# Kernel optimization log

Measured on AMD Instinct MI355X. Metric: run time of the kernel, lower is better.

Reference implementation:

```python
import jax, jax.numpy as jnp
import numpy as np

BIG_NUMBER = 1e7   # repo constant used to mask padded adjacency slots
MAX_ITERS = 32     # params['flow_iters']


def _build_graph(B, N, D, valid_deg, seed=0):
    """Random d-regular-ish graph: each valid slot d holds a permutation of nodes,
    so every node has exactly `valid_deg` in-edges. in_indices[b,v,d] = (b,u,s)
    such that adj[b,u,s] == v. Padded slots (d >= valid_deg) hold the sentinel N
    and their in_indices point to a padded (near-zero-weight) flow entry."""
    rng = np.random.default_rng(seed)
    adj = np.full((B, N, D), N, dtype=np.int32)
    in_idx = np.zeros((B, N, D, 3), dtype=np.int32)
    in_idx[..., 0] = np.arange(B, dtype=np.int32)[:, None, None]
    in_idx[..., 2] = valid_deg  # padded slots -> flow[b, 0, valid_deg] (weight ~ 0)
    for b in range(B):
        for d in range(valid_deg):
            perm = rng.permutation(N).astype(np.int32)
            adj[b, :, d] = perm                      # edge u -> perm[u] via slot d
            inv = np.argsort(perm).astype(np.int32)  # inv[v] = u with perm[u] == v
            in_idx[b, :, d, 1] = inv
            in_idx[b, :, d, 2] = d
    return jnp.asarray(adj), jnp.asarray(in_idx)


def setup_inputs():
    B, N, D, VALID = 4, 100000, 16, 12
    key = jax.random.key(0)
    k1, k2 = jax.random.split(key)
    adj_lst, in_indices = _build_graph(B, N, D, VALID)
    return {
        "flow_proportions": jax.random.normal(k1, (B, N, D), dtype=jnp.float32),
        "demands": jax.random.normal(k2, (B, N, 1), dtype=jnp.float32),
        "adj_lst": adj_lst,
        "in_indices": in_indices,
        "num_nodes": N,
    }


def reference(flow_proportions, demands, adj_lst, in_indices, num_nodes):
    # --- masked softmax over neighbor slots (padded slots get -BIG_NUMBER) ---
    mask = (adj_lst == num_nodes).astype(flow_proportions.dtype)   # [B,N,D]
    masked = flow_proportions - BIG_NUMBER * mask
    weights = jax.nn.softmax(masked, axis=-1)                      # normalized_weights

    # --- mcf_solver: iterate flow <- weights * relu(inflow - demand) ---
    bidx = in_indices[..., 0]   # [B,N,D] batch index
    src = in_indices[..., 1]    # [B,N,D] source node of d-th in-edge
    slot = in_indices[..., 2]   # [B,N,D] slot of this node in source's adj list

    def step(flow, _):
        # gather incoming edge flows, sum -> inflow per node [B,N,1]
        inflow = flow[bidx, src, slot].sum(axis=-1, keepdims=True)
        new_flow = weights * jax.nn.relu(inflow - demands)
        return new_flow, None

    flow, _ = jax.lax.scan(step, jnp.zeros_like(weights), None, length=MAX_ITERS)
    # flow_cost (loss) = sum over nodes/slots of cost_fn(flow) = flow**2 here:
    # flow_cost = jnp.sum(flow * flow, axis=(1, 2))
    return flow
```

## Files before the change

kernel.cpp:

```cpp
#include <hip/hip_runtime.h>

#define DEG 16
#define E12 12
#define MAX_ITERS 32
#define BLK 1024

__device__ __forceinline__ float ld_sc0(const float* p) {
    return __hip_atomic_load(p, __ATOMIC_RELAXED, __HIP_MEMORY_SCOPE_AGENT);
}
__device__ __forceinline__ void st_sc0(float* p, float v) {
    __hip_atomic_store(p, v, __ATOMIC_RELAXED, __HIP_MEMORY_SCOPE_AGENT);
}
__device__ __forceinline__ unsigned ld_u32_sc0(const unsigned* p) {
    return __hip_atomic_load(p, __ATOMIC_RELAXED, __HIP_MEMORY_SCOPE_AGENT);
}

__device__ __forceinline__ int get_xcd() {
    unsigned x;
    asm volatile("s_getreg_b32 %0, hwreg(HW_REG_XCC_ID)" : "=s"(x));
    return (int)(x & 7u);
}

__device__ __forceinline__ void grid_barrier(unsigned* cnt, unsigned* gen,
                                             unsigned target, unsigned nblocks) {
    __syncthreads();
    if (threadIdx.x == 0) {
        __threadfence();
        unsigned arrived = __hip_atomic_fetch_add(cnt, 1u, __ATOMIC_ACQ_REL,
                                                  __HIP_MEMORY_SCOPE_AGENT);
        if (arrived == nblocks - 1u) {
            __hip_atomic_store(cnt, 0u, __ATOMIC_RELAXED, __HIP_MEMORY_SCOPE_AGENT);
            __hip_atomic_fetch_add(gen, 1u, __ATOMIC_RELEASE, __HIP_MEMORY_SCOPE_AGENT);
        } else {
            while (__hip_atomic_load(gen, __ATOMIC_RELAXED,
                                     __HIP_MEMORY_SCOPE_AGENT) < target)
                __builtin_amdgcn_s_sleep(2);
        }
        __threadfence();
    }
    __syncthreads();
}

__device__ __forceinline__ void xcd_barrier(unsigned* cnt, unsigned* gen,
                                            unsigned target, unsigned nblocks) {
    __syncthreads();
    if (threadIdx.x == 0) {
        unsigned arrived = __hip_atomic_fetch_add(cnt, 1u, __ATOMIC_RELEASE,
                                                  __HIP_MEMORY_SCOPE_WORKGROUP);
        if (arrived == nblocks - 1u) {
            __hip_atomic_store(cnt, 0u, __ATOMIC_RELAXED,
                               __HIP_MEMORY_SCOPE_WORKGROUP);
            __hip_atomic_fetch_add(gen, 1u, __ATOMIC_RELEASE,
                                   __HIP_MEMORY_SCOPE_WORKGROUP);
        } else {
            while (ld_u32_sc0(gen) < target)
                __builtin_amdgcn_s_sleep(2);
        }
    }
    __syncthreads();
}

__device__ __forceinline__ void softmax_row(const float* __restrict__ fp,
                                            const int* __restrict__ adj,
                                            float* __restrict__ wout,
                                            size_t base, int N) {
    const float4* f4 = (const float4*)(fp + base);
    const int4*   a4 = (const int4*)(adj + base);
    float v[DEG];
#pragma unroll
    for (int k = 0; k < DEG / 4; ++k) {
        float4 f = f4[k];
        int4   a = a4[k];
        v[4*k+0] = (a.x == N) ? f.x - 1e7f : f.x;
        v[4*k+1] = (a.y == N) ? f.y - 1e7f : f.y;
        v[4*k+2] = (a.z == N) ? f.z - 1e7f : f.z;
        v[4*k+3] = (a.w == N) ? f.w - 1e7f : f.w;
    }
    float m = v[0];
#pragma unroll
    for (int j = 1; j < DEG; ++j) m = fmaxf(m, v[j]);
    float s = 0.f;
#pragma unroll
    for (int j = 0; j < DEG; ++j) { v[j] = __expf(v[j] - m); s += v[j]; }
    float inv = 1.f / s;
    float4* w4 = (float4*)(wout + base);
#pragma unroll
    for (int k = 0; k < DEG / 4; ++k) {
        float4 o;
        o.x = v[4*k+0] * inv;
        o.y = v[4*k+1] * inv;
        o.z = v[4*k+2] * inv;
        o.w = v[4*k+3] * inv;
        w4[k] = o;
    }
}

__device__ __forceinline__ float node_acc_sc0(const int* __restrict__ es,
                                              const float* __restrict__ ew,
                                              const float* __restrict__ Rc) {
    const int4*   s4 = (const int4*)es;
    const float4* w4 = (const float4*)ew;
    int4 a = s4[0], b = s4[1], c = s4[2];
    float4 x = w4[0], y = w4[1], z = w4[2];
    float acc;
    acc  = x.x * ld_sc0(Rc + a.x);
    acc += x.y * ld_sc0(Rc + a.y);
    acc += x.z * ld_sc0(Rc + a.z);
    acc += x.w * ld_sc0(Rc + a.w);
    acc += y.x * ld_sc0(Rc + b.x);
    acc += y.y * ld_sc0(Rc + b.y);
    acc += y.z * ld_sc0(Rc + b.z);
    acc += y.w * ld_sc0(Rc + b.w);
    acc += z.x * ld_sc0(Rc + c.x);
    acc += z.y * ld_sc0(Rc + c.y);
    acc += z.z * ld_sc0(Rc + c.z);
    acc += z.w * ld_sc0(Rc + c.w);
    return acc;
}

__device__ __forceinline__ float node_acc_plain(const int* __restrict__ es,
                                                const float* __restrict__ ew,
                                                const float* __restrict__ Rc) {
    const int4*   s4 = (const int4*)es;
    const float4* w4 = (const float4*)ew;
    int4 a = s4[0], b = s4[1], c = s4[2];
    float4 x = w4[0], y = w4[1], z = w4[2];
    float acc;
    acc  = x.x * Rc[a.x];
    acc += x.y * Rc[a.y];
    acc += x.z * Rc[a.z];
    acc += x.w * Rc[a.w];
    acc += y.x * Rc[b.x];
    acc += y.y * Rc[b.y];
    acc += y.z * Rc[b.z];
    acc += y.w * Rc[b.w];
    acc += z.x * Rc[c.x];
    acc += z.y * Rc[c.y];
    acc += z.z * Rc[c.z];
    acc += z.w * Rc[c.w];
    return acc;
}

__global__ __launch_bounds__(BLK, 8)
void fused6_k(const float* __restrict__ fp, const int* __restrict__ adj,
              const int* __restrict__ in_idx, const float* __restrict__ dem,
              const int* __restrict__ nn, float* __restrict__ wout,
              char* __restrict__ wsb, int nodes) {
    unsigned* g_cnt   = (unsigned*)(wsb);
    unsigned* g_gen   = (unsigned*)(wsb + 128);
    unsigned* blkcnt  = (unsigned*)(wsb + 2304);
    unsigned* ovf     = (unsigned*)(wsb + 2432);
    int*   e_src  = (int*)(wsb + 4096);
    float* e_w    = (float*)(wsb + 4096 + (size_t)E12 * nodes * 4);
    float* slices = e_w + (size_t)E12 * nodes;
    float* Rf     = slices + 4 * (size_t)nodes;

    const int N  = *nn;
    const int Nb = N;
    const unsigned nblocks = gridDim.x;
    const int tid = (int)threadIdx.x;

    __shared__ int sh_xcd, sh_rank, sh_mode, sh_K;
    unsigned gb = 0;

    if (tid == 0) {
        int x = get_xcd();
        sh_xcd  = x;
        sh_rank = (int)__hip_atomic_fetch_add(&blkcnt[x], 1u, __ATOMIC_RELAXED,
                                              __HIP_MEMORY_SCOPE_AGENT);
    }
    __syncthreads();
    const int my_xcd  = sh_xcd;
    const int my_rank = sh_rank;

    {
        int g = (int)blockIdx.x * BLK + tid;
        if (g < nodes) softmax_row(fp, adj, wout, (size_t)g * DEG, N);
    }
    grid_barrier(g_cnt, g_gen, ++gb, nblocks);

    if (tid == 0) {
        const int need = (Nb + 2 * BLK - 1) / (2 * BLK);
        unsigned c[8];
#pragma unroll
        for (int x = 0; x < 8; ++x) c[x] = ld_u32_sc0(&blkcnt[x]);
        bool ok = (4 * Nb == nodes) && (Nb > 0);
#pragma unroll
        for (int b = 0; b < 4; ++b)
            ok = ok && (c[2*b] >= (unsigned)need || c[2*b+1] >= (unsigned)need);
        sh_mode = ok ? 1 : 0;
        sh_K    = (int)c[my_xcd];
    }
    __syncthreads();

    {
        int g = (int)blockIdx.x * BLK + tid;
        if (g < nodes) {
            const int4* t4 = (const int4*)(in_idx + 3 * (size_t)g * DEG);
            int   cs[DEG]; float cw[DEG]; int cb[DEG];
#pragma unroll
            for (int q = 0; q < 4; ++q) {
                int4 qa = t4[3*q + 0];
                int4 qb = t4[3*q + 1];
                int4 qc = t4[3*q + 2];
                cb[4*q+0] = qa.x; cs[4*q+0] = qa.y; int l0 = qa.z;
                cb[4*q+1] = qa.w; cs[4*q+1] = qb.x; int l1 = qb.y;
                cb[4*q+2] = qb.z; cs[4*q+2] = qb.w; int l2 = qc.x;
                cb[4*q+3] = qc.y; cs[4*q+3] = qc.z; int l3 = qc.w;
                cw[4*q+0] = wout[((size_t)(cb[4*q+0]) * Nb + cs[4*q+0]) * DEG + l0];
                cw[4*q+1] = wout[((size_t)(cb[4*q+1]) * Nb + cs[4*q+1]) * DEG + l1];
                cw[4*q+2] = wout[((size_t)(cb[4*q+2]) * Nb + cs[4*q+2]) * DEG + l2];
                cw[4*q+3] = wout[((size_t)(cb[4*q+3]) * Nb + cs[4*q+3]) * DEG + l3];
            }
            const int gbatch = g / Nb;
            bool bad = (cw[12] != 0.f) || (cw[13] != 0.f) ||
                       (cw[14] != 0.f) || (cw[15] != 0.f);
#pragma unroll
            for (int k = 0; k < E12; ++k) bad = bad || (cb[k] != gbatch);
            if (bad)
                __hip_atomic_store(ovf, 1u, __ATOMIC_RELAXED,
                                   __HIP_MEMORY_SCOPE_AGENT);
            int4*   es4 = (int4*)(e_src + (size_t)g * E12);
            float4* ew4 = (float4*)(e_w + (size_t)g * E12);
            es4[0] = make_int4(cs[0], cs[1], cs[2], cs[3]);
            es4[1] = make_int4(cs[4], cs[5], cs[6], cs[7]);
            es4[2] = make_int4(cs[8], cs[9], cs[10], cs[11]);
            ew4[0] = make_float4(cw[0], cw[1], cw[2], cw[3]);
            ew4[1] = make_float4(cw[4], cw[5], cw[6], cw[7]);
            ew4[2] = make_float4(cw[8], cw[9], cw[10], cw[11]);
        }
    }
    grid_barrier(g_cnt, g_gen, ++gb, nblocks);

    if (tid == 0) {
        if (ld_u32_sc0(ovf) != 0u) sh_mode = 0;
    }
    __syncthreads();
    const bool fast = (sh_mode == 1);

    if (fast) {
        const int need = (Nb + 2 * BLK - 1) / (2 * BLK);
        const int K = sh_K;
        if (K < need) return;

        const int batch = my_xcd >> 1;
        const int bbase = batch * Nb;
        const int base  = my_rank * (2 * BLK);
        const int l0 = base + tid;
        const int l1 = base + tid + BLK;
        const bool a0 = (l0 < Nb), a1 = (l1 < Nb);
        const int g0 = bbase + l0, g1 = bbase + l1;

        unsigned* xc = (unsigned*)(wsb + 256 + my_xcd * 256);
        unsigned* xg = (unsigned*)(wsb + 256 + my_xcd * 256 + 128);
        unsigned xb = 0;

        float* R0s = slices + (size_t)(my_xcd * 2 + 0) * Nb;
        float* R1s = slices + (size_t)(my_xcd * 2 + 1) * Nb;

        float d0 = a0 ? dem[g0] : 0.f;
        float d1 = a1 ? dem[g1] : 0.f;

        float r0 = fmaxf(-d0, 0.f), r1 = fmaxf(-d1, 0.f);
        if (a0) st_sc0(R0s + l0, r0);
        if (a1) st_sc0(R1s + l1, r1);
        if (a0) st_sc0(R1s + l0, r0);
        if (a1) st_sc0(R0s + l1, r1);
        xcd_barrier(xc, xg, ++xb, (unsigned)K);

        const float* Rc = R0s;
        float*       Rn = R1s;
        const int* es0 = e_src + (size_t)g0 * E12;
        const int* es1 = e_src + (size_t)g1 * E12;
        const float* ew0 = e_w + (size_t)g0 * E12;
        const float* ew1 = e_w + (size_t)g1 * E12;

        for (int t = 1; t < MAX_ITERS; ++t) {
            if (a0) r0 = fmaxf(node_acc_sc0(es0, ew0, Rc) - d0, 0.f);
            if (a1) r1 = fmaxf(node_acc_sc0(es1, ew1, Rc) - d1, 0.f);
            if (t < MAX_ITERS - 1) {
                if (a0) st_sc0(Rn + l0, r0);
                if (a1) st_sc0(Rn + l1, r1);
                xcd_barrier(xc, xg, ++xb, (unsigned)K);
                const float* tmp = Rc; Rc = Rn; Rn = (float*)tmp;
            }
        }

        if (a0) {
            float4* w4 = (float4*)(wout + (size_t)g0 * DEG);
#pragma unroll
            for (int k = 0; k < DEG / 4; ++k) {
                float4 v = w4[k];
                v.x *= r0; v.y *= r0; v.z *= r0; v.w *= r0;
                w4[k] = v;
            }
        }
        if (a1) {
            float4* w4 = (float4*)(wout + (size_t)g1 * DEG);
#pragma unroll
            for (int k = 0; k < DEG / 4; ++k) {
                float4 v = w4[k];
                v.x *= r1; v.y *= r1; v.z *= r1; v.w *= r1;
                w4[k] = v;
            }
        }
    } else {
        const int g = (int)blockIdx.x * BLK + tid;
        const bool act = (g < nodes);
        int gbbase = 0;
        float d = 0.f;
        if (act) { gbbase = (g / Nb) * Nb; d = dem[g]; }
        const int*   es = e_src + (size_t)g * E12;
        const float* ew = e_w + (size_t)g * E12;

        float r = fmaxf(-d, 0.f);
        if (act) Rf[g] = r;
        grid_barrier(g_cnt, g_gen, ++gb, nblocks);

        const float* Rc = Rf;
        float*       Rn = Rf + nodes;
        for (int t = 1; t < MAX_ITERS; ++t) {
            if (act) r = fmaxf(node_acc_plain(es, ew, Rc + gbbase) - d, 0.f);
            if (t < MAX_ITERS - 1) {
                if (act) Rn[g] = r;
                grid_barrier(g_cnt, g_gen, ++gb, nblocks);
                const float* tmp = Rc; Rc = Rn; Rn = (float*)tmp;
            }
        }
        if (act) {
            float4* w4 = (float4*)(wout + (size_t)g * DEG);
#pragma unroll
            for (int k = 0; k < DEG / 4; ++k) {
                float4 v = w4[k];
                v.x *= r; v.y *= r; v.z *= r; v.w *= r;
                w4[k] = v;
            }
        }
    }
}

__global__ void softmax_k(const float* __restrict__ fp, const int* __restrict__ adj,
                          const int* __restrict__ nn, float* __restrict__ wout,
                          int nodes) {
    int i = blockIdx.x * blockDim.x + threadIdx.x;
    if (i >= nodes) return;
    softmax_row(fp, adj, wout, (size_t)i * DEG, *nn);
}

__global__ void gather_k(const int* __restrict__ in_idx, const float* __restrict__ w,
                         const int* __restrict__ nn, int* __restrict__ e_srcO,
                         float* __restrict__ e_wO, int edges) {
    int e = blockIdx.x * blockDim.x + threadIdx.x;
    if (e >= edges) return;
    const int N = *nn;
    size_t e3 = 3 * (size_t)e;
    int fi = in_idx[e3] * N + in_idx[e3 + 1];
    e_srcO[e] = fi;
    e_wO[e]   = w[(size_t)fi * DEG + in_idx[e3 + 2]];
}

__global__ void iter_k(const int* __restrict__ e_srcO, const float* __restrict__ e_wO,
                       const float* __restrict__ dem, const float* __restrict__ Rin,
                       float* __restrict__ Rout, int nodes) {
    int i = blockIdx.x * blockDim.x + threadIdx.x;
    if (i >= nodes) return;
    const size_t base = (size_t)i * DEG;
    const int4*   s4 = (const int4*)(e_srcO + base);
    const float4* w4 = (const float4*)(e_wO + base);
    float acc = 0.f;
#pragma unroll
    for (int k = 0; k < DEG / 4; ++k) {
        int4   s = s4[k];
        float4 w = w4[k];
        acc += w.x * Rin[s.x];
        acc += w.y * Rin[s.y];
        acc += w.z * Rin[s.z];
        acc += w.w * Rin[s.w];
    }
    float r = acc - dem[i];
    Rout[i] = r > 0.f ? r : 0.f;
}

__global__ void final_k(const float* __restrict__ w, const float* __restrict__ R,
                        float* __restrict__ out, int nodes) {
    int i = blockIdx.x * blockDim.x + threadIdx.x;
    if (i >= nodes) return;
    float r = R[i];
    const size_t base = (size_t)i * DEG;
    const float4* w4 = (const float4*)(w + base);
    float4* o4 = (float4*)(out + base);
#pragma unroll
    for (int k = 0; k < DEG / 4; ++k) {
        float4 v = w4[k];
        v.x *= r; v.y *= r; v.z *= r; v.w *= r;
        o4[k] = v;
    }
}

extern "C" void kernel_launch(void* const* d_in, const int* in_sizes, int n_in,
                              void* d_out, int out_size, void* d_ws, size_t ws_size,
                              hipStream_t stream) {
    const float* fp  = (const float*)d_in[0];
    const float* dem = (const float*)d_in[1];
    const int*   adj = (const int*)d_in[2];
    const int*   idx = (const int*)d_in[3];
    const int*   nn  = (const int*)d_in[4];

    const int edges = in_sizes[0];
    const int nodes = in_sizes[1];

    float* weights = (float*)d_out;
    char*  ws      = (char*)d_ws;

    int dev = 0, cus = 0, maxBlk = 0;
    hipGetDevice(&dev);
    hipDeviceGetAttribute(&cus, hipDeviceAttributeMultiprocessorCount, dev);
    hipOccupancyMaxActiveBlocksPerMultiprocessor(&maxBlk, (const void*)fused6_k,
                                                 BLK, 0);

    const int grid = 2 * cus;
    const size_t ws_need = 4096 + (size_t)nodes * (E12 * 8 + 16 + 8);

    const bool fused_ok = (maxBlk >= 2) &&
                          ((long long)grid * BLK >= nodes) &&
                          (ws_size >= ws_need) &&
                          (nodes % 4 == 0);

    if (fused_ok) {
        hipMemsetAsync(ws, 0, 4096, stream);
        void* args[] = { (void*)&fp, (void*)&adj, (void*)&idx, (void*)&dem,
                         (void*)&nn, (void*)&weights, (void*)&ws, (void*)&nodes };
        hipLaunchCooperativeKernel((const void*)fused6_k, dim3(grid), dim3(BLK),
                                   args, 0, stream);
    } else {
        int*   e_srcO = (int*)ws;
        float* e_wO   = (float*)(ws + (size_t)edges * sizeof(int));
        float* R0     = (float*)(ws + (size_t)edges * 8);
        float* R1     = R0 + nodes;
        const int blk = 256;
        const int gn = (nodes + blk - 1) / blk;
        const int ge = (edges + blk - 1) / blk;
        hipMemsetAsync(R0, 0, (size_t)nodes * sizeof(float), stream);
        softmax_k<<<gn, blk, 0, stream>>>(fp, adj, nn, weights, nodes);
        gather_k<<<ge, blk, 0, stream>>>(idx, weights, nn, e_srcO, e_wO, edges);
        float* a = R0;
        float* b = R1;
        for (int t = 0; t < MAX_ITERS; ++t) {
            iter_k<<<gn, blk, 0, stream>>>(e_srcO, e_wO, dem, a, b, nodes);
            float* tmp = a; a = b; b = tmp;
        }
        final_k<<<gn, blk, 0, stream>>>(weights, a, (float*)d_out, nodes);
    }
}
```

Baseline: 1.025 ms.

## Stage residual vector in LDS chunks with per-thread pre-binned edge lists

Reworks the persistent cooperative kernel to launch one block per CU, with 32 blocks per XCD each owning about 3125 nodes (4 per thread). Before iterating, each thread bins its 48 incoming edges by source chunk into a global region of packed (src|slot tag, weight) pairs. Each iteration streams the batch's residual vector through LDS in up to 4 chunks and accumulates from LDS instead of doing scattered global atomic-scope loads. The cost is extra LDS staging passes, per-chunk syncthreads, a large preprocessed edge region read every iteration, and lower occupancy.

```diff
diff --git a/kernel.cpp b/kernel.cpp
--- a/kernel.cpp
+++ b/kernel.cpp
@@ -4,15 +4,20 @@
 #define E12 12
 #define MAX_ITERS 32
 #define BLK 1024
+#define LDSF 25600
+#define JMAX 96
 
 __device__ __forceinline__ float ld_sc0(const float* p) {
-    return __hip_atomic_load(p, __ATOMIC_RELAXED, __HIP_MEMORY_SCOPE_AGENT);
+    return __hip_atomic_load((float*)p, __ATOMIC_RELAXED, __HIP_MEMORY_SCOPE_AGENT);
 }
 __device__ __forceinline__ void st_sc0(float* p, float v) {
     __hip_atomic_store(p, v, __ATOMIC_RELAXED, __HIP_MEMORY_SCOPE_AGENT);
 }
 __device__ __forceinline__ unsigned ld_u32_sc0(const unsigned* p) {
-    return __hip_atomic_load(p, __ATOMIC_RELAXED, __HIP_MEMORY_SCOPE_AGENT);
+    return __hip_atomic_load((unsigned*)p, __ATOMIC_RELAXED, __HIP_MEMORY_SCOPE_AGENT);
+}
+__device__ __forceinline__ void st_u32_sc0(unsigned* p, unsigned v) {
+    __hip_atomic_store(p, v, __ATOMIC_RELAXED, __HIP_MEMORY_SCOPE_AGENT);
 }
 
 __device__ __forceinline__ int get_xcd() {
@@ -95,247 +100,310 @@
     }
 }
 
-__device__ __forceinline__ float node_acc_sc0(const int* __restrict__ es,
-                                              const float* __restrict__ ew,
-                                              const float* __restrict__ Rc) {
+__device__ __forceinline__ float node_acc12(const int* __restrict__ es,
+                                            const float* __restrict__ ew,
+                                            const float* __restrict__ Rc) {
     const int4*   s4 = (const int4*)es;
     const float4* w4 = (const float4*)ew;
     int4 a = s4[0], b = s4[1], c = s4[2];
     float4 x = w4[0], y = w4[1], z = w4[2];
     float acc;
-    acc  = x.x * ld_sc0(Rc + a.x);
-    acc += x.y * ld_sc0(Rc + a.y);
-    acc += x.z * ld_sc0(Rc + a.z);
-    acc += x.w * ld_sc0(Rc + a.w);
-    acc += y.x * ld_sc0(Rc + b.x);
-    acc += y.y * ld_sc0(Rc + b.y);
-    acc += y.z * ld_sc0(Rc + b.z);
-    acc += y.w * ld_sc0(Rc + b.w);
-    acc += z.x * ld_sc0(Rc + c.x);
-    acc += z.y * ld_sc0(Rc + c.y);
-    acc += z.z * ld_sc0(Rc + c.z);
-    acc += z.w * ld_sc0(Rc + c.w);
+    acc  = x.x * Rc[a.x];  acc += x.y * Rc[a.y];
+    acc += x.z * Rc[a.z];  acc += x.w * Rc[a.w];
+    acc += y.x * Rc[b.x];  acc += y.y * Rc[b.y];
+    acc += y.z * Rc[b.z];  acc += y.w * Rc[b.w];
+    acc += z.x * Rc[c.x];  acc += z.y * Rc[c.y];
+    acc += z.z * Rc[c.z];  acc += z.w * Rc[c.w];
     return acc;
 }
 
-__device__ __forceinline__ float node_acc_plain(const int* __restrict__ es,
-                                                const float* __restrict__ ew,
-                                                const float* __restrict__ Rc) {
-    const int4*   s4 = (const int4*)es;
-    const float4* w4 = (const float4*)ew;
-    int4 a = s4[0], b = s4[1], c = s4[2];
-    float4 x = w4[0], y = w4[1], z = w4[2];
-    float acc;
-    acc  = x.x * Rc[a.x];
-    acc += x.y * Rc[a.y];
-    acc += x.z * Rc[a.z];
-    acc += x.w * Rc[a.w];
-    acc += y.x * Rc[b.x];
-    acc += y.y * Rc[b.y];
-    acc += y.z * Rc[b.z];
-    acc += y.w * Rc[b.w];
-    acc += z.x * Rc[c.x];
-    acc += z.y * Rc[c.y];
-    acc += z.z * Rc[c.z];
-    acc += z.w * Rc[c.w];
-    return acc;
-}
-
-__global__ __launch_bounds__(BLK, 8)
-void fused6_k(const float* __restrict__ fp, const int* __restrict__ adj,
+__device__ __forceinline__ void scale_row(float* __restrict__ wout, int g, float r) {
+    float4* w4 = (float4*)(wout + (size_t)g * DEG);
+#pragma unroll
+    for (int k = 0; k < DEG / 4; ++k) {
+        float4 v = w4[k];
+        v.x *= r; v.y *= r; v.z *= r; v.w *= r;
+        w4[k] = v;
+    }
+}
+
+__global__ __launch_bounds__(BLK, 4)
+void fused7_k(const float* __restrict__ fp, const int* __restrict__ adj,
               const int* __restrict__ in_idx, const float* __restrict__ dem,
               const int* __restrict__ nn, float* __restrict__ wout,
               char* __restrict__ wsb, int nodes) {
-    unsigned* g_cnt   = (unsigned*)(wsb);
-    unsigned* g_gen   = (unsigned*)(wsb + 128);
-    unsigned* blkcnt  = (unsigned*)(wsb + 2304);
-    unsigned* ovf     = (unsigned*)(wsb + 2432);
-    int*   e_src  = (int*)(wsb + 4096);
-    float* e_w    = (float*)(wsb + 4096 + (size_t)E12 * nodes * 4);
-    float* slices = e_w + (size_t)E12 * nodes;
-    float* Rf     = slices + 4 * (size_t)nodes;
-
-    const int N  = *nn;
-    const int Nb = N;
+    __shared__ float lds[LDSF];
+    __shared__ int s_xcd, s_rank, s_mode, s_part, s_jbad;
+    __shared__ int s_cm[4];
+    __shared__ int s_off[5];
+
+    unsigned* g_cnt  = (unsigned*)(wsb);
+    unsigned* g_gen  = (unsigned*)(wsb + 128);
+    unsigned* blkcnt = (unsigned*)(wsb + 2304);
+    unsigned* ovf    = (unsigned*)(wsb + 2432);
+    unsigned* jovf   = (unsigned*)(wsb + 2436);
+    int*   e_src   = (int*)(wsb + 4096);
+    float* e_w     = (float*)(wsb + 4096 + (size_t)nodes * E12 * 4);
+    float* Rf0     = (float*)((char*)e_w + (size_t)nodes * E12 * 4);
+    float* Rf1     = Rf0 + nodes;
+    float* slices  = Rf1 + nodes;
+    uint2* regions = (uint2*)((char*)(slices) + (size_t)nodes * 16);
+
+    const int N   = *nn;
+    const int tid = (int)threadIdx.x;
+    const int T   = (int)gridDim.x * BLK;
     const unsigned nblocks = gridDim.x;
-    const int tid = (int)threadIdx.x;
-
-    __shared__ int sh_xcd, sh_rank, sh_mode, sh_K;
     unsigned gb = 0;
 
     if (tid == 0) {
         int x = get_xcd();
-        sh_xcd  = x;
-        sh_rank = (int)__hip_atomic_fetch_add(&blkcnt[x], 1u, __ATOMIC_RELAXED,
-                                              __HIP_MEMORY_SCOPE_AGENT);
+        s_xcd  = x;
+        s_rank = (int)__hip_atomic_fetch_add(&blkcnt[x], 1u, __ATOMIC_RELAXED,
+                                             __HIP_MEMORY_SCOPE_AGENT);
     }
     __syncthreads();
-    const int my_xcd  = sh_xcd;
-    const int my_rank = sh_rank;
+    const int my_xcd  = s_xcd;
+    const int my_rank = s_rank;
+
+#pragma unroll
+    for (int rep = 0; rep < 2; ++rep) {
+        int g = (int)blockIdx.x * BLK + tid + rep * T;
+        if (g < nodes) softmax_row(fp, adj, wout, (size_t)g * DEG, N);
+    }
+    grid_barrier(g_cnt, g_gen, ++gb, nblocks);
+
+#pragma unroll
+    for (int rep = 0; rep < 2; ++rep) {
+        int g = (int)blockIdx.x * BLK + tid + rep * T;
+        if (g >= nodes) continue;
+        const int gbat = g / N;
+        const int4* t4 = (const int4*)(in_idx + (size_t)g * 48);
+        int cb[16], cs[16], cl[16];
+#pragma unroll
+        for (int q = 0; q < 4; ++q) {
+            int4 qa = t4[3*q + 0];
+            int4 qb = t4[3*q + 1];
+            int4 qc = t4[3*q + 2];
+            cb[4*q+0] = qa.x; cs[4*q+0] = qa.y; cl[4*q+0] = qa.z;
+            cb[4*q+1] = qa.w; cs[4*q+1] = qb.x; cl[4*q+1] = qb.y;
+            cb[4*q+2] = qb.z; cs[4*q+2] = qb.w; cl[4*q+2] = qc.x;
+            cb[4*q+3] = qc.y; cs[4*q+3] = qc.z; cl[4*q+3] = qc.w;
+        }
+        float cw[16];
+#pragma unroll
+        for (int k = 0; k < 16; ++k)
+            cw[k] = wout[((size_t)cb[k] * N + cs[k]) * DEG + cl[k]];
+        bool bad = (cw[12] != 0.f) || (cw[13] != 0.f) ||
+                   (cw[14] != 0.f) || (cw[15] != 0.f);
+#pragma unroll
+        for (int k = 0; k < E12; ++k)
+            bad = bad || (cb[k] != gbat) || ((unsigned)cs[k] >= (unsigned)N);
+        if (bad) st_u32_sc0(ovf, 1u);
+        int4*   es4 = (int4*)(e_src + (size_t)g * E12);
+        float4* ew4 = (float4*)(e_w + (size_t)g * E12);
+        es4[0] = make_int4(cs[0], cs[1], cs[2], cs[3]);
+        es4[1] = make_int4(cs[4], cs[5], cs[6], cs[7]);
+        es4[2] = make_int4(cs[8], cs[9], cs[10], cs[11]);
+        ew4[0] = make_float4(cw[0], cw[1], cw[2], cw[3]);
+        ew4[1] = make_float4(cw[4], cw[5], cw[6], cw[7]);
+        ew4[2] = make_float4(cw[8], cw[9], cw[10], cw[11]);
+    }
+    grid_barrier(g_cnt, g_gen, ++gb, nblocks);
+
+    const int npb   = (N + 31) >> 5;
+    const int nch   = (N + LDSF - 1) / LDSF;
+    const int chunk = (N + nch - 1) / nch;
+    if (tid == 0) {
+        unsigned cc[8];
+#pragma unroll
+        for (int x = 0; x < 8; ++x) cc[x] = ld_u32_sc0(&blkcnt[x]);
+        bool ok = (4 * N == nodes) && (N > 0) && (npb <= 4 * BLK) &&
+                  (nch >= 1) && (nch <= 4) && (chunk <= LDSF) &&
+                  (ld_u32_sc0(ovf) == 0u);
+#pragma unroll
+        for (int p = 0; p < 4; ++p)
+            ok = ok && (cc[2*p] >= 32u || cc[2*p+1] >= 32u);
+        s_mode = ok ? 1 : 0;
+        s_part = (ok && cc[my_xcd] >= 32u && my_rank < 32) ? 1 : 0;
+    }
+    __syncthreads();
+    const bool fast = (s_mode == 1);
+    const bool part = (s_part == 1);
+
+    if (fast) {
+        const int batch = my_xcd >> 1;
+        const int lbase = my_rank * npb;
+        const int lim   = min(lbase + npb, N);
+        float d[4];
+        int   lno[4];
+        bool  act[4];
+        float r[4];
+        uint2* reg = regions + (size_t)(my_xcd * 32 + my_rank) * (JMAX * BLK);
+
+        if (part) {
+            if (tid < 4) s_cm[tid] = 0;
+            __syncthreads();
+            const int b1 = chunk, b2 = 2 * chunk, b3 = 3 * chunk;
+            int c0 = 0, c1 = 0, c2 = 0, c3 = 0;
+#pragma unroll
+            for (int s = 0; s < 4; ++s) {
+                int l = lbase + s * BLK + tid;
+                lno[s] = l;
+                act[s] = (l < lim);
+                d[s] = 0.f;
+                if (act[s]) {
+                    int g = batch * N + l;
+                    d[s] = dem[g];
+                    const int* es = e_src + (size_t)g * E12;
+#pragma unroll
+                    for (int k = 0; k < E12; ++k) {
+                        int src = es[k];
+                        int c = (src >= b1) + (src >= b2) + (src >= b3);
+                        c0 += (c == 0); c1 += (c == 1);
+                        c2 += (c == 2); c3 += (c == 3);
+                    }
+                }
+            }
+            atomicMax(&s_cm[0], c0); atomicMax(&s_cm[1], c1);
+            atomicMax(&s_cm[2], c2); atomicMax(&s_cm[3], c3);
+            __syncthreads();
+            if (tid == 0) {
+                s_off[0] = 0;
+                s_off[1] = s_cm[0];
+                s_off[2] = s_cm[0] + s_cm[1];
+                s_off[3] = s_cm[0] + s_cm[1] + s_cm[2];
+                s_off[4] = s_cm[0] + s_cm[1] + s_cm[2] + s_cm[3];
+                if (s_off[4] > JMAX) st_u32_sc0(jovf, 1u);
+            }
+            __syncthreads();
+            if (s_off[4] <= JMAX) {
+                int cur0 = s_off[0], cur1 = s_off[1],
+                    cur2 = s_off[2], cur3 = s_off[3];
+#pragma unroll
+                for (int s = 0; s < 4; ++s) {
+                    if (!act[s]) continue;
+                    int g = batch * N + lno[s];
+                    const int*   es = e_src + (size_t)g * E12;
+                    const float* ew = e_w + (size_t)g * E12;
+#pragma unroll
+                    for (int k = 0; k < E12; ++k) {
+                        int src = es[k];
+                        float w = ew[k];
+                        int c = (src >= b1) + (src >= b2) + (src >= b3);
+                        int j = (c == 0) ? cur0 : (c == 1) ? cur1
+                               : (c == 2) ? cur2 : cur3;
+                        reg[(size_t)j * BLK + tid] =
+                            make_uint2((unsigned)src | ((unsigned)s << 20),
+                                       __float_as_uint(w));
+                        cur0 += (c == 0); cur1 += (c == 1);
+                        cur2 += (c == 2); cur3 += (c == 3);
+                    }
+                }
+                int curs[1];
+                (void)curs;
+                {
+                    int cc_[4] = {cur0, cur1, cur2, cur3};
+#pragma unroll
+                    for (int c = 0; c < 4; ++c) {
+                        unsigned ps = (unsigned)(c * chunk);
+                        for (int j = cc_[c]; j < s_off[c + 1]; ++j)
+                            reg[(size_t)j * BLK + tid] = make_uint2(ps, 0u);
+                    }
+                }
+            }
+        }
+        grid_barrier(g_cnt, g_gen, ++gb, nblocks);
+        if (tid == 0) s_jbad = (int)ld_u32_sc0(jovf);
+        __syncthreads();
+
+        if (s_jbad == 0) {
+            if (!part) return;
+            unsigned* xc = (unsigned*)(wsb + 256 + my_xcd * 256);
+            unsigned* xg = (unsigned*)(wsb + 256 + my_xcd * 256 + 128);
+            unsigned xb = 0;
+            float* bufA = slices + (size_t)(2 * my_xcd + 0) * N;
+            float* bufB = slices + (size_t)(2 * my_xcd + 1) * N;
+
+#pragma unroll
+            for (int s = 0; s < 4; ++s) {
+                r[s] = fmaxf(-d[s], 0.f);
+                if (act[s]) st_sc0(bufA + lno[s], r[s]);
+            }
+            xcd_barrier(xc, xg, ++xb, 32u);
+
+            float* Rin  = bufA;
+            float* Rout = bufB;
+            for (int t = 1; t < MAX_ITERS; ++t) {
+                float a0 = 0.f, a1 = 0.f, a2 = 0.f, a3 = 0.f;
+                for (int c = 0; c < nch; ++c) {
+                    const int cbase = c * chunk;
+                    const int ce = min(chunk, N - cbase);
+                    for (int i = tid; i < ce; i += BLK)
+                        lds[i] = ld_sc0(Rin + cbase + i);
+                    __syncthreads();
+                    const int jb = s_off[c], je = s_off[c + 1];
+                    for (int j = jb; j < je; ++j) {
+                        uint2 pr = reg[(size_t)j * BLK + tid];
+                        float w = __uint_as_float(pr.y);
+                        int idx = (int)(pr.x & 0xFFFFFu) - cbase;
+                        int tg  = (int)(pr.x >> 20);
+                        float wv = w * lds[idx];
+                        a0 += (tg == 0) ? wv : 0.f;
+                        a1 += (tg == 1) ? wv : 0.f;
+                        a2 += (tg == 2) ? wv : 0.f;
+                        a3 += (tg == 3) ? wv : 0.f;
+                    }
+                    __syncthreads();
+                }
+                r[0] = fmaxf(a0 - d[0], 0.f);
+                r[1] = fmaxf(a1 - d[1], 0.f);
+                r[2] = fmaxf(a2 - d[2], 0.f);
+                r[3] = fmaxf(a3 - d[3], 0.f);
+                if (t < MAX_ITERS - 1) {
+#pragma unroll
+                    for (int s = 0; s < 4; ++s)
+                        if (act[s]) st_sc0(Rout + lno[s], r[s]);
+                    xcd_barrier(xc, xg, ++xb, 32u);
+                    float* tmp = Rin; Rin = Rout; Rout = tmp;
+                }
+            }
+#pragma unroll
+            for (int s = 0; s < 4; ++s)
+                if (act[s]) scale_row(wout, batch * N + lno[s], r[s]);
+            return;
+        }
+    }
 
     {
-        int g = (int)blockIdx.x * BLK + tid;
-        if (g < nodes) softmax_row(fp, adj, wout, (size_t)g * DEG, N);
-    }
-    grid_barrier(g_cnt, g_gen, ++gb, nblocks);
-
-    if (tid == 0) {
-        const int need = (Nb + 2 * BLK - 1) / (2 * BLK);
-        unsigned c[8];
-#pragma unroll
-        for (int x = 0; x < 8; ++x) c[x] = ld_u32_sc0(&blkcnt[x]);
-        bool ok = (4 * Nb == nodes) && (Nb > 0);
-#pragma unroll
-        for (int b = 0; b < 4; ++b)
-            ok = ok && (c[2*b] >= (unsigned)need || c[2*b+1] >= (unsigned)need);
-        sh_mode = ok ? 1 : 0;
-        sh_K    = (int)c[my_xcd];
-    }
-    __syncthreads();
-
-    {
-        int g = (int)blockIdx.x * BLK + tid;
-        if (g < nodes) {
-            const int4* t4 = (const int4*)(in_idx + 3 * (size_t)g * DEG);
-            int   cs[DEG]; float cw[DEG]; int cb[DEG];
-#pragma unroll
-            for (int q = 0; q < 4; ++q) {
-                int4 qa = t4[3*q + 0];
-                int4 qb = t4[3*q + 1];
-                int4 qc = t4[3*q + 2];
-                cb[4*q+0] = qa.x; cs[4*q+0] = qa.y; int l0 = qa.z;
-                cb[4*q+1] = qa.w; cs[4*q+1] = qb.x; int l1 = qb.y;
-                cb[4*q+2] = qb.z; cs[4*q+2] = qb.w; int l2 = qc.x;
-                cb[4*q+3] = qc.y; cs[4*q+3] = qc.z; int l3 = qc.w;
-                cw[4*q+0] = wout[((size_t)(cb[4*q+0]) * Nb + cs[4*q+0]) * DEG + l0];
-                cw[4*q+1] = wout[((size_t)(cb[4*q+1]) * Nb + cs[4*q+1]) * DEG + l1];
-                cw[4*q+2] = wout[((size_t)(cb[4*q+2]) * Nb + cs[4*q+2]) * DEG + l2];
-                cw[4*q+3] = wout[((size_t)(cb[4*q+3]) * Nb + cs[4*q+3]) * DEG + l3];
-            }
-            const int gbatch = g / Nb;
-            bool bad = (cw[12] != 0.f) || (cw[13] != 0.f) ||
-                       (cw[14] != 0.f) || (cw[15] != 0.f);
-#pragma unroll
-            for (int k = 0; k < E12; ++k) bad = bad || (cb[k] != gbatch);
-            if (bad)
-                __hip_atomic_store(ovf, 1u, __ATOMIC_RELAXED,
-                                   __HIP_MEMORY_SCOPE_AGENT);
-            int4*   es4 = (int4*)(e_src + (size_t)g * E12);
-            float4* ew4 = (float4*)(e_w + (size_t)g * E12);
-            es4[0] = make_int4(cs[0], cs[1], cs[2], cs[3]);
-            es4[1] = make_int4(cs[4], cs[5], cs[6], cs[7]);
-            es4[2] = make_int4(cs[8], cs[9], cs[10], cs[11]);
-            ew4[0] = make_float4(cw[0], cw[1], cw[2], cw[3]);
-            ew4[1] = make_float4(cw[4], cw[5], cw[6], cw[7]);
-            ew4[2] = make_float4(cw[8], cw[9], cw[10], cw[11]);
-        }
-    }
-    grid_barrier(g_cnt, g_gen, ++gb, nblocks);
-
-    if (tid == 0) {
-        if (ld_u32_sc0(ovf) != 0u) sh_mode = 0;
-    }
-    __syncthreads();
-    const bool fast = (sh_mode == 1);
-
-    if (fast) {
-        const int need = (Nb + 2 * BLK - 1) / (2 * BLK);
-        const int K = sh_K;
-        if (K < need) return;
-
-        const int batch = my_xcd >> 1;
-        const int bbase = batch * Nb;
-        const int base  = my_rank * (2 * BLK);
-        const int l0 = base + tid;
-        const int l1 = base + tid + BLK;
-        const bool a0 = (l0 < Nb), a1 = (l1 < Nb);
-        const int g0 = bbase + l0, g1 = bbase + l1;
-
-        unsigned* xc = (unsigned*)(wsb + 256 + my_xcd * 256);
-        unsigned* xg = (unsigned*)(wsb + 256 + my_xcd * 256 + 128);
-        unsigned xb = 0;
-
-        float* R0s = slices + (size_t)(my_xcd * 2 + 0) * Nb;
-        float* R1s = slices + (size_t)(my_xcd * 2 + 1) * Nb;
-
+        int g0 = (int)blockIdx.x * BLK + tid;
+        int g1 = g0 + T;
+        bool a0 = (g0 < nodes), a1 = (g1 < nodes);
         float d0 = a0 ? dem[g0] : 0.f;
         float d1 = a1 ? dem[g1] : 0.f;
-
+        int base0 = a0 ? (g0 / N) * N : 0;
+        int base1 = a1 ? (g1 / N) * N : 0;
         float r0 = fmaxf(-d0, 0.f), r1 = fmaxf(-d1, 0.f);
-        if (a0) st_sc0(R0s + l0, r0);
-        if (a1) st_sc0(R1s + l1, r1);
-        if (a0) st_sc0(R1s + l0, r0);
-        if (a1) st_sc0(R0s + l1, r1);
-        xcd_barrier(xc, xg, ++xb, (unsigned)K);
-
-        const float* Rc = R0s;
-        float*       Rn = R1s;
-        const int* es0 = e_src + (size_t)g0 * E12;
-        const int* es1 = e_src + (size_t)g1 * E12;
-        const float* ew0 = e_w + (size_t)g0 * E12;
-        const float* ew1 = e_w + (size_t)g1 * E12;
-
+        if (a0) Rf0[g0] = r0;
+        if (a1) Rf0[g1] = r1;
+        grid_barrier(g_cnt, g_gen, ++gb, nblocks);
+        const float* Rc = Rf0;
+        float*       Rn = Rf1;
         for (int t = 1; t < MAX_ITERS; ++t) {
-            if (a0) r0 = fmaxf(node_acc_sc0(es0, ew0, Rc) - d0, 0.f);
-            if (a1) r1 = fmaxf(node_acc_sc0(es1, ew1, Rc) - d1, 0.f);
+            if (a0) r0 = fmaxf(node_acc12(e_src + (size_t)g0 * E12,
+                                          e_w + (size_t)g0 * E12,
+                                          Rc + base0) - d0, 0.f);
+            if (a1) r1 = fmaxf(node_acc12(e_src + (size_t)g1 * E12,
+                                          e_w + (size_t)g1 * E12,
+                                          Rc + base1) - d1, 0.f);
             if (t < MAX_ITERS - 1) {
-                if (a0) st_sc0(Rn + l0, r0);
-                if (a1) st_sc0(Rn + l1, r1);
-                xcd_barrier(xc, xg, ++xb, (unsigned)K);
-                const float* tmp = Rc; Rc = Rn; Rn = (float*)tmp;
+                if (a0) Rn[g0] = r0;
+                if (a1) Rn[g1] = r1;
+                grid_barrier(g_cnt, g_gen, ++gb, nblocks);
+                float* tmp = (float*)Rc; Rc = Rn; Rn = tmp;
             }
         }
-
-        if (a0) {
-            float4* w4 = (float4*)(wout + (size_t)g0 * DEG);
-#pragma unroll
-            for (int k = 0; k < DEG / 4; ++k) {
-                float4 v = w4[k];
-                v.x *= r0; v.y *= r0; v.z *= r0; v.w *= r0;
-                w4[k] = v;
-            }
-        }
-        if (a1) {
-            float4* w4 = (float4*)(wout + (size_t)g1 * DEG);
-#pragma unroll
-            for (int k = 0; k < DEG / 4; ++k) {
-                float4 v = w4[k];
-                v.x *= r1; v.y *= r1; v.z *= r1; v.w *= r1;
-                w4[k] = v;
-            }
-        }
-    } else {
-        const int g = (int)blockIdx.x * BLK + tid;
-        const bool act = (g < nodes);
-        int gbbase = 0;
-        float d = 0.f;
-        if (act) { gbbase = (g / Nb) * Nb; d = dem[g]; }
-        const int*   es = e_src + (size_t)g * E12;
-        const float* ew = e_w + (size_t)g * E12;
-
-        float r = fmaxf(-d, 0.f);
-        if (act) Rf[g] = r;
-        grid_barrier(g_cnt, g_gen, ++gb, nblocks);
-
-        const float* Rc = Rf;
-        float*       Rn = Rf + nodes;
-        for (int t = 1; t < MAX_ITERS; ++t) {
-            if (act) r = fmaxf(node_acc_plain(es, ew, Rc + gbbase) - d, 0.f);
-            if (t < MAX_ITERS - 1) {
-                if (act) Rn[g] = r;
-                grid_barrier(g_cnt, g_gen, ++gb, nblocks);
-                const float* tmp = Rc; Rc = Rn; Rn = (float*)tmp;
-            }
-        }
-        if (act) {
-            float4* w4 = (float4*)(wout + (size_t)g * DEG);
-#pragma unroll
-            for (int k = 0; k < DEG / 4; ++k) {
-                float4 v = w4[k];
-                v.x *= r; v.y *= r; v.z *= r; v.w *= r;
-                w4[k] = v;
-            }
-        }
+        if (a0) scale_row(wout, g0, r0);
+        if (a1) scale_row(wout, g1, r1);
     }
 }
 
@@ -385,16 +453,8 @@
                         float* __restrict__ out, int nodes) {
     int i = blockIdx.x * blockDim.x + threadIdx.x;
     if (i >= nodes) return;
-    float r = R[i];
-    const size_t base = (size_t)i * DEG;
-    const float4* w4 = (const float4*)(w + base);
-    float4* o4 = (float4*)(out + base);
-#pragma unroll
-    for (int k = 0; k < DEG / 4; ++k) {
-        float4 v = w4[k];
-        v.x *= r; v.y *= r; v.z *= r; v.w *= r;
-        o4[k] = v;
-    }
+    scale_row((float*)w, i, R[i]);
+    (void)out;
 }
 
 extern "C" void kernel_launch(void* const* d_in, const int* in_sizes, int n_in,
@@ -415,22 +475,22 @@
     int dev = 0, cus = 0, maxBlk = 0;
     hipGetDevice(&dev);
     hipDeviceGetAttribute(&cus, hipDeviceAttributeMultiprocessorCount, dev);
-    hipOccupancyMaxActiveBlocksPerMultiprocessor(&maxBlk, (const void*)fused6_k,
+    hipOccupancyMaxActiveBlocksPerMultiprocessor(&maxBlk, (const void*)fused7_k,
                                                  BLK, 0);
 
-    const int grid = 2 * cus;
-    const size_t ws_need = 4096 + (size_t)nodes * (E12 * 8 + 16 + 8);
-
-    const bool fused_ok = (maxBlk >= 2) &&
-                          ((long long)grid * BLK >= nodes) &&
-                          (ws_size >= ws_need) &&
-                          (nodes % 4 == 0);
+    const size_t need = 4096 + (size_t)nodes * (E12 * 8 + 8 + 16)
+                      + (size_t)256 * JMAX * BLK * 8;
+    const int grid = cus;
+
+    const bool fused_ok = (maxBlk >= 1) && (cus >= 16) &&
+                          ((long long)grid * BLK * 2 >= nodes) &&
+                          (ws_size >= need) && (nodes % 4 == 0);
 
     if (fused_ok) {
         hipMemsetAsync(ws, 0, 4096, stream);
         void* args[] = { (void*)&fp, (void*)&adj, (void*)&idx, (void*)&dem,
                          (void*)&nn, (void*)&weights, (void*)&ws, (void*)&nodes };
-        hipLaunchCooperativeKernel((const void*)fused6_k, dim3(grid), dim3(BLK),
+        hipLaunchCooperativeKernel((const void*)fused7_k, dim3(grid), dim3(BLK),
                                    args, 0, stream);
     } else {
         int*   e_srcO = (int*)ws;
```

New measurement: 1.024 ms. Within noise of the previous version (-0.1%).
